# Performance work log

Hardware: AMD Instinct MI355X
Metric: run time of the kernel (lower is better)

## Reference

```python
import jax, jax.numpy as jnp
import numpy as np

B, T, C, H = 4, 2048, 1024, 16
D = C // H


def setup_inputs() -> dict:
    key = jax.random.key(0)
    ks = jax.random.split(key, 6)
    s = 1.0 / np.sqrt(C)
    return {
        "x": jax.random.normal(ks[0], (B, T, C), dtype=jnp.float32),
        "attention_mask": jnp.ones((B, 1, T), dtype=jnp.int32),
        "Wq": jax.random.normal(ks[1], (C, C), dtype=jnp.float32) * s,
        "bq": jnp.zeros((C,), dtype=jnp.float32),
        "Wk": jax.random.normal(ks[2], (C, C), dtype=jnp.float32) * s,
        "bk": jnp.zeros((C,), dtype=jnp.float32),
        "Wv": jax.random.normal(ks[3], (C, C), dtype=jnp.float32) * s,
        "bv": jnp.zeros((C,), dtype=jnp.float32),
        "Wp": jax.random.normal(ks[4], (C, C), dtype=jnp.float32) * s,
        "bp": jnp.zeros((C,), dtype=jnp.float32),
    }


def reference(x, attention_mask, Wq, bq, Wk, bk, Wv, bv, Wp, bp):
    b, t, c = x.shape
    d = c // H
    # projections (torch Linear: x @ W^T + b)
    q = (x @ Wq.T + bq).reshape(b, t, H, d).transpose(0, 2, 1, 3)  # [B,H,T,D]
    k = (x @ Wk.T + bk).reshape(b, t, H, d).transpose(0, 2, 1, 3)
    v = (x @ Wv.T + bv).reshape(b, t, H, d).transpose(0, 2, 1, 3)
    attn = jnp.einsum("bhqd,bhkd->bhqk", q, k) / jnp.sqrt(jnp.asarray(d, x.dtype))
    mask = attention_mask[:, :, :t]  # [B,1,T] -> broadcast over [B,H,T,T] keys
    attn = jnp.where(mask[:, :, None, :] == 0, jnp.asarray(-jnp.inf, x.dtype), attn)
    attn = jax.nn.softmax(attn, axis=-1)  # dropout p=0 (eval)
    y = jnp.einsum("bhqk,bhkd->bhqd", attn, v)
    y = y.transpose(0, 2, 1, 3).reshape(b, t, c)
    return y @ Wp.T + bp
```

## Files before the change

### kernel.cpp

```cpp
#include <hip/hip_runtime.h>


#define TT 2048
#define CC 1024
#define HH 16
#define DD 64
#define BB 4

typedef unsigned short u16;
typedef unsigned int u32;
typedef __attribute__((ext_vector_type(8))) short bf16x8;
typedef __attribute__((ext_vector_type(4))) float f32x4;
typedef __attribute__((ext_vector_type(4))) u32 u32x4;

#if __has_builtin(__builtin_amdgcn_exp2f)
#define EXP2(x) __builtin_amdgcn_exp2f(x)
#else
#define EXP2(x) __expf((x) * 0.6931471805599453f)
#endif

__device__ __forceinline__ u16 f2bf(float f) {
    u32 u = __builtin_bit_cast(u32, f);
    u += 0x7FFFu + ((u >> 16) & 1u);
    return (u16)(u >> 16);
}
__device__ __forceinline__ u32 pk2(float a, float b) {
    u32 ua = __builtin_bit_cast(u32, a); ua += 0x7FFFu + ((ua >> 16) & 1u);
    u32 ub = __builtin_bit_cast(u32, b); ub += 0x7FFFu + ((ub >> 16) & 1u);
    return __builtin_amdgcn_perm(ub, ua, 0x07060302);
}
__device__ __forceinline__ u32 cvtpk(float lo, float hi) {
    u32 r;
    asm("v_cvt_pk_bf16_f32 %0, %1, %2" : "=v"(r) : "v"(lo), "v"(hi));
    return r;
}

#define GLDS(g, l) __builtin_amdgcn_global_load_lds( \
    (const __attribute__((address_space(1))) void*)(g), \
    (__attribute__((address_space(3))) void*)(l), 16, 0, 0)

#define PH_SYNC() { __builtin_amdgcn_sched_barrier(0); \
                    __builtin_amdgcn_s_barrier(); \
                    __builtin_amdgcn_sched_barrier(0); }

__global__ __launch_bounds__(256) void wcvt(const float* __restrict__ s,
                                            u16* __restrict__ d, int n8) {
    const int i = blockIdx.x * 256 + threadIdx.x;
    if (i < n8) {
        const float4 f0 = ((const float4*)s)[2 * i];
        const float4 f1 = ((const float4*)s)[2 * i + 1];
        uint4 w;
        w.x = pk2(f0.x, f0.y); w.y = pk2(f0.z, f0.w);
        w.z = pk2(f1.x, f1.y); w.w = pk2(f1.z, f1.w);
        ((uint4*)d)[i] = w;
    }
}

__global__ __launch_bounds__(256) void wcvtA(const float* __restrict__ x,
                                             const float* __restrict__ Wq,
                                             const float* __restrict__ Wk,
                                             const float* __restrict__ Wv,
                                             u16* __restrict__ xb,
                                             u16* __restrict__ Wq16,
                                             u16* __restrict__ Wk16,
                                             u16* __restrict__ Wv16) {
    const int bid = blockIdx.x;
    const float* s; u16* d; int i;
    if (bid < 4096) {
        s = x; d = xb; i = bid * 256 + threadIdx.x;
    } else {
        const int t = bid - 4096;
        const int which = t >> 9, sub = t & 511;
        s = (which == 0) ? Wq : (which == 1) ? Wk : Wv;
        d = (which == 0) ? Wq16 : (which == 1) ? Wk16 : Wv16;
        i = sub * 256 + threadIdx.x;
    }
    const float4 f0 = ((const float4*)s)[2 * i];
    const float4 f1 = ((const float4*)s)[2 * i + 1];
    uint4 w;
    w.x = pk2(f0.x, f0.y); w.y = pk2(f0.z, f0.w);
    w.z = pk2(f1.x, f1.y); w.w = pk2(f1.z, f1.w);
    ((uint4*)d)[i] = w;
}

__global__ __launch_bounds__(512) void gemm8p(const u16* __restrict__ Ag,
                                              const u16* __restrict__ Wb,
                                              const float* __restrict__ b0,
                                              const float* __restrict__ b1,
                                              const float* __restrict__ b2,
                                              u16* __restrict__ outQ,
                                              u16* __restrict__ outK,
                                              u16* __restrict__ outV) {
    extern __shared__ u16 lds[];
    const int tid  = threadIdx.x;
    const int wave = tid >> 6, lane = tid & 63;
    const int quad = lane >> 4, l16 = lane & 15;
    const int wr = wave >> 2, wc = wave & 3;
    constexpr int NT = CC / 64;

    const int bid0 = blockIdx.y * 12 + blockIdx.x;
    const int bid  = (bid0 & 7) * 48 + (bid0 >> 3);
    const int bn = (bid % 12) * 256, bm = (bid / 12) * 256;

    u32 aOff[4], bOff[4]; int dstOff[4];
#pragma unroll
    for (int g = 0; g < 4; g++) {
        const int c = g * 512 + tid;
        const int row = c >> 3;
        const int kc = (c & 7) ^ (row & 7);
        aOff[g] = (u32)(bm + row) * CC + kc * 8;
        bOff[g] = (u32)(bn + row) * CC + kc * 8;
        dstOff[g] = c * 8;
    }

    int aO[8], bO[4];
#pragma unroll
    for (int i = 0; i < 8; i++) {
        const int row = wr * 128 + i * 16 + l16;
        aO[i] = row * 64 + (quad ^ (row & 7)) * 8;
    }
#pragma unroll
    for (int j = 0; j < 4; j++) {
        const int row = wc * 64 + j * 16 + l16;
        bO[j] = row * 64 + (quad ^ (row & 7)) * 8;
    }

    f32x4 acc[8][4] = {};

    {
        u16* An = lds;
        u16* Bn = lds + 32768;
        GLDS(&Ag[(size_t)aOff[0]], &An[dstOff[0]]);
        GLDS(&Ag[(size_t)aOff[2]], &An[dstOff[2]]);
#pragma unroll
        for (int g = 0; g < 4; g++) GLDS(&Wb[(size_t)bOff[g]], &Bn[dstOff[g]]);
        GLDS(&Ag[(size_t)aOff[1]], &An[dstOff[1]]);
        GLDS(&Ag[(size_t)aOff[3]], &An[dstOff[3]]);
        asm volatile("s_waitcnt vmcnt(2)" ::: "memory");
        PH_SYNC();
    }

#pragma unroll 1
    for (int t = 0; t < NT; t++) {
        const u16* Ab = lds + (t & 1) * 16384;
        const u16* Bb = lds + 32768 + (t & 1) * 16384;
        u16* An = lds + ((t & 1) ^ 1) * 16384;
        u16* Bn = lds + 32768 + ((t & 1) ^ 1) * 16384;
        const int k1 = (t + 1) * 64;
        const bool pf = (t + 1 < NT);

        bf16x8 af[4], bfr[4];

#pragma unroll
        for (int j = 0; j < 4; j++) bfr[j] = *(const bf16x8*)&Bb[bO[j]];
#pragma unroll
        for (int i = 0; i < 4; i++) af[i] = *(const bf16x8*)&Ab[aO[i]];
        asm volatile("s_waitcnt lgkmcnt(0)" ::: "memory");
        __builtin_amdgcn_sched_barrier(0);
        __builtin_amdgcn_s_setprio(1);
#pragma unroll
        for (int i = 0; i < 4; i++)
#pragma unroll
            for (int j = 0; j < 4; j++)
                acc[i][j] = __builtin_amdgcn_mfma_f32_16x16x32_bf16(af[i], bfr[j], acc[i][j], 0, 0, 0);
        __builtin_amdgcn_s_setprio(0);
        asm volatile("s_waitcnt vmcnt(0)" ::: "memory");
        PH_SYNC();

        if (pf) {
            GLDS(&Ag[(size_t)aOff[0] + k1], &An[dstOff[0]]);
            GLDS(&Ag[(size_t)aOff[2] + k1], &An[dstOff[2]]);
        }
#pragma unroll
        for (int i = 0; i < 4; i++) af[i] = *(const bf16x8*)&Ab[aO[4 + i]];
        asm volatile("s_waitcnt lgkmcnt(0)" ::: "memory");
        __builtin_amdgcn_sched_barrier(0);
        __builtin_amdgcn_s_setprio(1);
#pragma unroll
        for (int i = 0; i < 4; i++)
#pragma unroll
            for (int j = 0; j < 4; j++)
                acc[4 + i][j] = __builtin_amdgcn_mfma_f32_16x16x32_bf16(af[i], bfr[j], acc[4 + i][j], 0, 0, 0);
        __builtin_amdgcn_s_setprio(0);
        PH_SYNC();

        if (pf) {
#pragma unroll
            for (int g = 0; g < 4; g++)
                GLDS(&Wb[(size_t)bOff[g] + k1], &Bn[dstOff[g]]);
        }
#pragma unroll
        for (int j = 0; j < 4; j++) bfr[j] = *(const bf16x8*)&Bb[bO[j] ^ 32];
#pragma unroll
        for (int i = 0; i < 4; i++) af[i] = *(const bf16x8*)&Ab[aO[i] ^ 32];
        asm volatile("s_waitcnt lgkmcnt(0)" ::: "memory");
        __builtin_amdgcn_sched_barrier(0);
        __builtin_amdgcn_s_setprio(1);
#pragma unroll
        for (int i = 0; i < 4; i++)
#pragma unroll
            for (int j = 0; j < 4; j++)
                acc[i][j] = __builtin_amdgcn_mfma_f32_16x16x32_bf16(af[i], bfr[j], acc[i][j], 0, 0, 0);
        __builtin_amdgcn_s_setprio(0);
        PH_SYNC();

        if (pf) {
            GLDS(&Ag[(size_t)aOff[1] + k1], &An[dstOff[1]]);
            GLDS(&Ag[(size_t)aOff[3] + k1], &An[dstOff[3]]);
        }
#pragma unroll
        for (int i = 0; i < 4; i++) af[i] = *(const bf16x8*)&Ab[aO[4 + i] ^ 32];
        asm volatile("s_waitcnt lgkmcnt(0)" ::: "memory");
        __builtin_amdgcn_sched_barrier(0);
        __builtin_amdgcn_s_setprio(1);
#pragma unroll
        for (int i = 0; i < 4; i++)
#pragma unroll
            for (int j = 0; j < 4; j++)
                acc[4 + i][j] = __builtin_amdgcn_mfma_f32_16x16x32_bf16(af[i], bfr[j], acc[4 + i][j], 0, 0, 0);
        __builtin_amdgcn_s_setprio(0);
        if (pf) asm volatile("s_waitcnt vmcnt(2)" ::: "memory");
        else    asm volatile("s_waitcnt vmcnt(0)" ::: "memory");
        PH_SYNC();
    }

    const int mid = bn >> 10;
    const float* bias = (mid == 0) ? b0 : (mid == 1) ? b1 : b2;
#pragma unroll
    for (int j = 0; j < 4; j++) {
        const int col  = bn + wc * 64 + j * 16 + l16;
        const int colL = col & (CC - 1);
        const float bv = bias[colL];
#pragma unroll
        for (int i = 0; i < 8; i++) {
            const int row0 = bm + wr * 128 + i * 16 + quad * 4;
            if (mid < 2) {
                u16* out = mid ? outK : outQ;
#pragma unroll
                for (int r = 0; r < 4; r++)
                    out[(size_t)(row0 + r) * CC + colL] = f2bf(acc[i][j][r] + bv);
            } else {
                const int hh = colL >> 6, dch = colL & 63;
                const int bb = row0 >> 11, t0 = row0 & (TT - 1);
                const size_t idx = (((size_t)bb * HH + hh) * DD + dch) * TT + t0;
                uint2 w;
                w.x = pk2(acc[i][j][0] + bv, acc[i][j][1] + bv);
                w.y = pk2(acc[i][j][2] + bv, acc[i][j][3] + bv);
                *(uint2*)&outV[idx] = w;
            }
        }
    }
}

template <int BN, int WM, int WN, int MODE>
__global__ __launch_bounds__(512, 4) void gemmT(const u16* __restrict__ Ag,
                                                const u16* __restrict__ Bg,
                                                const float* __restrict__ b0,
                                                float* __restrict__ outF) {
    constexpr int NI = WM / 16, NJ = WN / 16;
    constexpr int WAVES_N = BN / WN;
    constexpr int BUFSZ = (256 + BN) * 32;
    constexpr int SPT = 2 + BN / 128;
    constexpr int NT = CC / 32;

    extern __shared__ u16 lds[];
    const int tid  = threadIdx.x;
    const int wave = tid >> 6, lane = tid & 63;
    const int quad = lane >> 4, l16 = lane & 15;
    const int wr = wave / WAVES_N, wc = wave & (WAVES_N - 1);

    constexpr int NBX = 1024 / BN;
    const int bid0 = blockIdx.y * NBX + blockIdx.x;
    const int chunk = (NBX * 32) >> 3;
    const int bid  = (bid0 & 7) * chunk + (bid0 >> 3);
    const int bn = (bid % NBX) * BN, bm = (bid / NBX) * 256;

    u32 aOff[2]; int aDst[2];
#pragma unroll
    for (int g = 0; g < 2; g++) {
        const int c = g * 512 + tid;
        const int row = c >> 2;
        const int kc = (c & 3) ^ ((row >> 1) & 3);
        aOff[g] = (u32)(bm + row) * CC + kc * 8;
        aDst[g] = c * 8;
    }
    u32 bOff[BN / 128]; int bDst[BN / 128];
#pragma unroll
    for (int g = 0; g < BN / 128; g++) {
        const int c = g * 512 + tid;
        const int row = c >> 2;
        const int kc = (c & 3) ^ ((row >> 1) & 3);
        bOff[g] = (u32)(bn + row) * CC + kc * 8;
        bDst[g] = 8192 + c * 8;
    }

    int aRd[NI], bRd[NJ];
#pragma unroll
    for (int i = 0; i < NI; i++) {
        const int row = wr * WM + i * 16 + l16;
        aRd[i] = row * 32 + (quad ^ ((row >> 1) & 3)) * 8;
    }
#pragma unroll
    for (int j = 0; j < NJ; j++) {
        const int row = wc * WN + j * 16 + l16;
        bRd[j] = 8192 + row * 32 + (quad ^ ((row >> 1) & 3)) * 8;
    }

    f32x4 acc[NI][NJ] = {};

#define STAGE_T(t)                                                        \
    {                                                                     \
        u16* dst = &lds[((t) % 3) * BUFSZ];                               \
        const int k0 = (t) * 32;                                          \
        _Pragma("unroll")                                                 \
        for (int g = 0; g < 2; g++)                                       \
            GLDS(&Ag[(size_t)aOff[g] + k0], &dst[aDst[g]]);               \
        _Pragma("unroll")                                                 \
        for (int g = 0; g < BN / 128; g++)                                \
            GLDS(&Bg[(size_t)bOff[g] + k0], &dst[bDst[g]]);               \
    }

#define COMPUTE_T(t)                                                      \
    {                                                                     \
        const u16* buf = &lds[((t) % 3) * BUFSZ];                         \
        bf16x8 af[NI], bfr[NJ];                                           \
        _Pragma("unroll")                                                 \
        for (int i = 0; i < NI; i++) af[i] = *(const bf16x8*)&buf[aRd[i]];\
        _Pragma("unroll")                                                 \
        for (int j = 0; j < NJ; j++) bfr[j] = *(const bf16x8*)&buf[bRd[j]];\
        __builtin_amdgcn_s_setprio(1);                                    \
        _Pragma("unroll")                                                 \
        for (int i = 0; i < NI; i++)                                      \
            _Pragma("unroll")                                             \
            for (int j = 0; j < NJ; j++)                                  \
                acc[i][j] = __builtin_amdgcn_mfma_f32_16x16x32_bf16(      \
                    af[i], bfr[j], acc[i][j], 0, 0, 0);                   \
        __builtin_amdgcn_s_setprio(0);                                    \
    }

#define WAIT_MAIN()                                                       \
    if constexpr (SPT == 3) asm volatile("s_waitcnt vmcnt(3)" ::: "memory"); \
    else                    asm volatile("s_waitcnt vmcnt(4)" ::: "memory");

    STAGE_T(0); STAGE_T(1);
    WAIT_MAIN();
    PH_SYNC();

#pragma unroll 1
    for (int t = 0; t < NT - 2; t++) {
        STAGE_T(t + 2);
        COMPUTE_T(t);
        WAIT_MAIN();
        PH_SYNC();
    }
    COMPUTE_T(NT - 2);
    asm volatile("s_waitcnt vmcnt(0)" ::: "memory");
    PH_SYNC();
    COMPUTE_T(NT - 1);

#undef STAGE_T
#undef COMPUTE_T
#undef WAIT_MAIN

#pragma unroll
    for (int j = 0; j < NJ; j++) {
        const int col = bn + wc * WN + j * 16 + l16;
        const float bv = b0[col];
#pragma unroll
        for (int i = 0; i < NI; i++) {
            const int row0 = bm + wr * WM + i * 16 + quad * 4;
#pragma unroll
            for (int r = 0; r < 4; r++)
                outF[(size_t)(row0 + r) * CC + col] = acc[i][j][r] + bv;
        }
    }
}

__global__ __launch_bounds__(512) void attn(const u16* __restrict__ Q,
                                            const u16* __restrict__ Kb,
                                            const u16* __restrict__ Vt,
                                            const int* __restrict__ mask,
                                            u16* __restrict__ Y) {
    const int b = blockIdx.z, h = blockIdx.y, qt = blockIdx.x;
    const int tid  = threadIdx.x;
    const int wave = tid >> 6, lane = tid & 63;
    const int quad = lane >> 4, l16 = lane & 15;
    const int qrow0 = qt * 256 + wave * 32;

    __shared__ u16 Ks[2][64 * 64];
    __shared__ u16 Vs[2][64 * 64];
    __shared__ __align__(16) float bias_lds[TT];

    const size_t qb = ((size_t)b * TT + qrow0) * CC + h * DD;

    bf16x8 qf[2][2];
#pragma unroll
    for (int m = 0; m < 2; m++)
#pragma unroll
        for (int ks = 0; ks < 2; ks++)
            qf[m][ks] = *(const bf16x8*)&Q[qb + (size_t)(m * 16 + l16) * CC + ks * 32 + quad * 8];

    {
        const int i = tid * 4;
        const int4 m0 = *(const int4*)&mask[b * TT + i];
        bias_lds[i + 0] = m0.x ? 0.f : -1e38f;
        bias_lds[i + 1] = m0.y ? 0.f : -1e38f;
        bias_lds[i + 2] = m0.z ? 0.f : -1e38f;
        bias_lds[i + 3] = m0.w ? 0.f : -1e38f;
    }

    const int c0 = tid;
    const int r0 = c0 >> 3;
    const int kp0 = (c0 & 7) ^ ((((r0 >> 3) & 1) << 2) | (r0 & 3));
    const int vp0 = (c0 & 7) ^ (r0 & 7);
    const u16* kgp = Kb + ((size_t)b * TT) * CC + h * DD;
    const u16* vgp = Vt + ((size_t)(b * HH + h) * DD) * TT;

    const int rowA = ((l16 >> 2) << 3) | (l16 & 3);
    const int s0k  = (((l16 >> 2) & 1) << 2) | (l16 & 3);

    f32x4 o[2][4] = {};
    float lsum[2] = {};
    const float SC = 0.18033688011112042f;

    GLDS(&kgp[(size_t)r0 * CC + kp0 * 8], &Ks[0][c0 * 8]);
    GLDS(&vgp[(size_t)r0 * TT + vp0 * 8], &Vs[0][c0 * 8]);
    asm volatile("s_waitcnt vmcnt(0) lgkmcnt(0)" ::: "memory");
    __builtin_amdgcn_s_barrier();
    __builtin_amdgcn_sched_barrier(0);

#pragma unroll 1
    for (int kt = 0; kt < TT; kt += 64) {
        const int cur = (kt >> 6) & 1;
        const u16* Kc = &Ks[cur][0];
        const u16* Vc = &Vs[cur][0];

        if (kt + 64 < TT) {
            const int nxt = cur ^ 1;
            GLDS(&kgp[(size_t)(kt + 64 + r0) * CC + kp0 * 8], &Ks[nxt][c0 * 8]);
            GLDS(&vgp[(size_t)r0 * TT + kt + 64 + vp0 * 8], &Vs[nxt][c0 * 8]);
        }

        const f32x4 bA = *(const f32x4*)&bias_lds[kt + quad * 8];
        const f32x4 bB = *(const f32x4*)&bias_lds[kt + quad * 8 + 4];
        const f32x4 bC = *(const f32x4*)&bias_lds[kt + 32 + quad * 8];
        const f32x4 bD = *(const f32x4*)&bias_lds[kt + 32 + quad * 8 + 4];

        f32x4 s2[2][4] = {};
        __builtin_amdgcn_s_setprio(1);
#pragma unroll
        for (int n = 0; n < 4; n++) {
            const int rowK = rowA + (n & 1) * 4 + (n >> 1) * 32;
#pragma unroll
            for (int ks = 0; ks < 2; ks++) {
                const int pos = ((ks << 2) + quad) ^ s0k;
                const bf16x8 kf = *(const bf16x8*)&Kc[rowK * 64 + pos * 8];
#pragma unroll
                for (int m = 0; m < 2; m++)
                    s2[m][n] = __builtin_amdgcn_mfma_f32_16x16x32_bf16(kf, qf[m][ks], s2[m][n], 0, 0, 0);
            }
        }
        __builtin_amdgcn_s_setprio(0);

#pragma unroll
        for (int ks = 0; ks < 2; ks++) {
            bf16x8 pf[2];
#pragma unroll
            for (int m = 0; m < 2; m++) {
                u32 pw[4];
#pragma unroll
                for (int nn = 0; nn < 2; nn++) {
                    const int n = 2 * ks + nn;
                    const f32x4 bv = (n == 0) ? bA : (n == 1) ? bB : (n == 2) ? bC : bD;
                    const float p0 = EXP2(fmaf(s2[m][n][0], SC, bv[0]));
                    const float p1 = EXP2(fmaf(s2[m][n][1], SC, bv[1]));
                    const float p2 = EXP2(fmaf(s2[m][n][2], SC, bv[2]));
                    const float p3 = EXP2(fmaf(s2[m][n][3], SC, bv[3]));
                    lsum[m] += (p0 + p1) + (p2 + p3);
                    pw[2 * nn]     = cvtpk(p0, p1);
                    pw[2 * nn + 1] = cvtpk(p2, p3);
                }
                const u32x4 t = { pw[0], pw[1], pw[2], pw[3] };
                pf[m] = __builtin_bit_cast(bf16x8, t);
            }
            __builtin_amdgcn_s_setprio(1);
#pragma unroll
            for (int dt = 0; dt < 4; dt++) {
                const int vrow = dt * 16 + l16;
                const int pos = ((ks << 2) + quad) ^ (vrow & 7);
                const bf16x8 vf = *(const bf16x8*)&Vc[vrow * 64 + pos * 8];
#pragma unroll
                for (int m = 0; m < 2; m++)
                    o[m][dt] = __builtin_amdgcn_mfma_f32_16x16x32_bf16(pf[m], vf, o[m][dt], 0, 0, 0);
            }
            __builtin_amdgcn_s_setprio(0);
        }

        asm volatile("s_waitcnt vmcnt(0)" ::: "memory");
        __builtin_amdgcn_sched_barrier(0);
        __builtin_amdgcn_s_barrier();
    }

#pragma unroll
    for (int m = 0; m < 2; m++) {
        lsum[m] += __shfl_xor(lsum[m], 16, 64);
        lsum[m] += __shfl_xor(lsum[m], 32, 64);
    }

#pragma unroll
    for (int m = 0; m < 2; m++) {
        float inv[4];
#pragma unroll
        for (int r = 0; r < 4; r++)
            inv[r] = 1.0f / __shfl(lsum[m], quad * 4 + r, 64);
#pragma unroll
        for (int dt = 0; dt < 4; dt++)
#pragma unroll
            for (int r = 0; r < 4; r++)
                Y[qb + (size_t)(m * 16 + quad * 4 + r) * CC + dt * 16 + l16] = f2bf(o[m][dt][r] * inv[r]);
    }
}

extern "C" void kernel_launch(void* const* d_in, const int* in_sizes, int n_in,
                              void* d_out, int out_size, void* d_ws, size_t ws_size,
                              hipStream_t stream) {
    const float* x    = (const float*)d_in[0];
    const int*   mask = (const int*)d_in[1];
    const float* Wq   = (const float*)d_in[2];
    const float* bq   = (const float*)d_in[3];
    const float* Wk   = (const float*)d_in[4];
    const float* bk   = (const float*)d_in[5];
    const float* Wv   = (const float*)d_in[6];
    const float* bv   = (const float*)d_in[7];
    const float* Wp   = (const float*)d_in[8];
    const float* bp   = (const float*)d_in[9];

    u16* ws = (u16*)d_ws;
    const size_t sz = (size_t)BB * TT * CC;
    u16* Qb   = ws;
    u16* Kbuf = ws + sz;
    u16* Vtb  = ws + 2 * sz;

    u16* xb   = (u16*)d_out;
    u16* Wq16 = xb + sz;
    u16* Wk16 = Wq16 + (size_t)CC * CC;
    u16* Wv16 = Wk16 + (size_t)CC * CC;

    static bool inited = false;
    if (!inited) {
        (void)hipFuncSetAttribute((const void*)gemm8p,
                                  hipFuncAttributeMaxDynamicSharedMemorySize, 131072);
        (void)hipFuncSetAttribute((const void*)gemmT<128, 64, 64, 1>,
                                  hipFuncAttributeMaxDynamicSharedMemorySize, 73728);
        inited = true;
    }

    const int W8 = CC * CC / 8;

    wcvtA<<<5632, 256, 0, stream>>>(x, Wq, Wk, Wv, xb, Wq16, Wk16, Wv16);

    gemm8p<<<dim3(12, 32), 512, 131072, stream>>>(
        xb, Wq16, bq, bk, bv, Qb, Kbuf, Vtb);

    attn<<<dim3(TT / 256, HH, BB), 512, 0, stream>>>(Qb, Kbuf, Vtb, mask, Qb);

    wcvt<<<512, 256, 0, stream>>>(Wp, Kbuf, W8);

    gemmT<128, 64, 64, 1><<<dim3(8, 32), 512, 73728, stream>>>(
        Qb, Kbuf, bp, (float*)d_out);
}
```

Before: 291.1 us.

## Issue QKV GEMM prefetch at iteration start and shrink output-projection tile

The fused QKV GEMM now issues all next-tile global-to-LDS loads at the start of each K iteration instead of spreading them across four phases. It waits for them all only at the end of the iteration. The output-projection GEMM is generalized with a BM parameter and launched with 128x128 tiles (512 blocks, 48KB LDS) instead of 256x128 (256 blocks). This gives more blocks for occupancy and load balance on the final projection, at the cost of less data reuse per block. Issuing the prefetch in one burst may also change the overlap with MFMA work.

```diff
diff --git a/kernel.cpp b/kernel.cpp
--- a/kernel.cpp
+++ b/kernel.cpp
@@ -83,7 +83,7 @@
     ((uint4*)d)[i] = w;
 }
 
-__global__ __launch_bounds__(512) void gemm8p(const u16* __restrict__ Ag,
+__global__ __launch_bounds__(512) void gemm4p(const u16* __restrict__ Ag,
                                               const u16* __restrict__ Wb,
                                               const float* __restrict__ b0,
                                               const float* __restrict__ b1,
@@ -130,13 +130,11 @@
     {
         u16* An = lds;
         u16* Bn = lds + 32768;
-        GLDS(&Ag[(size_t)aOff[0]], &An[dstOff[0]]);
-        GLDS(&Ag[(size_t)aOff[2]], &An[dstOff[2]]);
+#pragma unroll
+        for (int g = 0; g < 4; g++) GLDS(&Ag[(size_t)aOff[g]], &An[dstOff[g]]);
 #pragma unroll
         for (int g = 0; g < 4; g++) GLDS(&Wb[(size_t)bOff[g]], &Bn[dstOff[g]]);
-        GLDS(&Ag[(size_t)aOff[1]], &An[dstOff[1]]);
-        GLDS(&Ag[(size_t)aOff[3]], &An[dstOff[3]]);
-        asm volatile("s_waitcnt vmcnt(2)" ::: "memory");
+        asm volatile("s_waitcnt vmcnt(0)" ::: "memory");
         PH_SYNC();
     }
 
@@ -151,6 +149,14 @@
 
         bf16x8 af[4], bfr[4];
 
+        if (pf) {
+#pragma unroll
+            for (int g = 0; g < 4; g++)
+                GLDS(&Ag[(size_t)aOff[g] + k1], &An[dstOff[g]]);
+#pragma unroll
+            for (int g = 0; g < 4; g++)
+                GLDS(&Wb[(size_t)bOff[g] + k1], &Bn[dstOff[g]]);
+        }
 #pragma unroll
         for (int j = 0; j < 4; j++) bfr[j] = *(const bf16x8*)&Bb[bO[j]];
 #pragma unroll
@@ -164,13 +170,8 @@
             for (int j = 0; j < 4; j++)
                 acc[i][j] = __builtin_amdgcn_mfma_f32_16x16x32_bf16(af[i], bfr[j], acc[i][j], 0, 0, 0);
         __builtin_amdgcn_s_setprio(0);
-        asm volatile("s_waitcnt vmcnt(0)" ::: "memory");
         PH_SYNC();
 
-        if (pf) {
-            GLDS(&Ag[(size_t)aOff[0] + k1], &An[dstOff[0]]);
-            GLDS(&Ag[(size_t)aOff[2] + k1], &An[dstOff[2]]);
-        }
 #pragma unroll
         for (int i = 0; i < 4; i++) af[i] = *(const bf16x8*)&Ab[aO[4 + i]];
         asm volatile("s_waitcnt lgkmcnt(0)" ::: "memory");
@@ -184,11 +185,6 @@
         __builtin_amdgcn_s_setprio(0);
         PH_SYNC();
 
-        if (pf) {
-#pragma unroll
-            for (int g = 0; g < 4; g++)
-                GLDS(&Wb[(size_t)bOff[g] + k1], &Bn[dstOff[g]]);
-        }
 #pragma unroll
         for (int j = 0; j < 4; j++) bfr[j] = *(const bf16x8*)&Bb[bO[j] ^ 32];
 #pragma unroll
@@ -204,10 +200,6 @@
         __builtin_amdgcn_s_setprio(0);
         PH_SYNC();
 
-        if (pf) {
-            GLDS(&Ag[(size_t)aOff[1] + k1], &An[dstOff[1]]);
-            GLDS(&Ag[(size_t)aOff[3] + k1], &An[dstOff[3]]);
-        }
 #pragma unroll
         for (int i = 0; i < 4; i++) af[i] = *(const bf16x8*)&Ab[aO[4 + i] ^ 32];
         asm volatile("s_waitcnt lgkmcnt(0)" ::: "memory");
@@ -219,8 +211,7 @@
             for (int j = 0; j < 4; j++)
                 acc[4 + i][j] = __builtin_amdgcn_mfma_f32_16x16x32_bf16(af[i], bfr[j], acc[4 + i][j], 0, 0, 0);
         __builtin_amdgcn_s_setprio(0);
-        if (pf) asm volatile("s_waitcnt vmcnt(2)" ::: "memory");
-        else    asm volatile("s_waitcnt vmcnt(0)" ::: "memory");
+        asm volatile("s_waitcnt vmcnt(0)" ::: "memory");
         PH_SYNC();
     }
 
@@ -252,46 +243,49 @@
     }
 }
 
-template <int BN, int WM, int WN, int MODE>
+template <int BM, int BN, int WM, int WN>
 __global__ __launch_bounds__(512, 4) void gemmT(const u16* __restrict__ Ag,
                                                 const u16* __restrict__ Bg,
                                                 const float* __restrict__ b0,
                                                 float* __restrict__ outF) {
     constexpr int NI = WM / 16, NJ = WN / 16;
     constexpr int WAVES_N = BN / WN;
-    constexpr int BUFSZ = (256 + BN) * 32;
-    constexpr int SPT = 2 + BN / 128;
+    constexpr int BOFF = BM * 32;
+    constexpr int BUFSZ = (BM + BN) * 32;
+    constexpr int AG = BM / 128, BG = BN / 128;
+    constexpr int SPT = AG + BG;
     constexpr int NT = CC / 32;
+    constexpr int NBX = 1024 / BN;
+    constexpr int NBY = 8192 / BM;
 
     extern __shared__ u16 lds[];
     const int tid  = threadIdx.x;
     const int wave = tid >> 6, lane = tid & 63;
     const int quad = lane >> 4, l16 = lane & 15;
-    const int wr = wave / WAVES_N, wc = wave & (WAVES_N - 1);
-
-    constexpr int NBX = 1024 / BN;
+    const int wr = wave / WAVES_N, wc = wave % WAVES_N;
+
     const int bid0 = blockIdx.y * NBX + blockIdx.x;
-    const int chunk = (NBX * 32) >> 3;
+    const int chunk = (NBX * NBY) >> 3;
     const int bid  = (bid0 & 7) * chunk + (bid0 >> 3);
-    const int bn = (bid % NBX) * BN, bm = (bid / NBX) * 256;
-
-    u32 aOff[2]; int aDst[2];
-#pragma unroll
-    for (int g = 0; g < 2; g++) {
+    const int bn = (bid % NBX) * BN, bm = (bid / NBX) * BM;
+
+    u32 aOff[AG]; int aDst[AG];
+#pragma unroll
+    for (int g = 0; g < AG; g++) {
         const int c = g * 512 + tid;
         const int row = c >> 2;
         const int kc = (c & 3) ^ ((row >> 1) & 3);
         aOff[g] = (u32)(bm + row) * CC + kc * 8;
         aDst[g] = c * 8;
     }
-    u32 bOff[BN / 128]; int bDst[BN / 128];
-#pragma unroll
-    for (int g = 0; g < BN / 128; g++) {
+    u32 bOff[BG]; int bDst[BG];
+#pragma unroll
+    for (int g = 0; g < BG; g++) {
         const int c = g * 512 + tid;
         const int row = c >> 2;
         const int kc = (c & 3) ^ ((row >> 1) & 3);
         bOff[g] = (u32)(bn + row) * CC + kc * 8;
-        bDst[g] = 8192 + c * 8;
+        bDst[g] = BOFF + c * 8;
     }
 
     int aRd[NI], bRd[NJ];
@@ -303,7 +297,7 @@
 #pragma unroll
     for (int j = 0; j < NJ; j++) {
         const int row = wc * WN + j * 16 + l16;
-        bRd[j] = 8192 + row * 32 + (quad ^ ((row >> 1) & 3)) * 8;
+        bRd[j] = BOFF + row * 32 + (quad ^ ((row >> 1) & 3)) * 8;
     }
 
     f32x4 acc[NI][NJ] = {};
@@ -313,10 +307,10 @@
         u16* dst = &lds[((t) % 3) * BUFSZ];                               \
         const int k0 = (t) * 32;                                          \
         _Pragma("unroll")                                                 \
-        for (int g = 0; g < 2; g++)                                       \
+        for (int g = 0; g < AG; g++)                                      \
             GLDS(&Ag[(size_t)aOff[g] + k0], &dst[aDst[g]]);               \
         _Pragma("unroll")                                                 \
-        for (int g = 0; g < BN / 128; g++)                                \
+        for (int g = 0; g < BG; g++)                                      \
             GLDS(&Bg[(size_t)bOff[g] + k0], &dst[bDst[g]]);               \
     }
 
@@ -339,8 +333,9 @@
     }
 
 #define WAIT_MAIN()                                                       \
-    if constexpr (SPT == 3) asm volatile("s_waitcnt vmcnt(3)" ::: "memory"); \
-    else                    asm volatile("s_waitcnt vmcnt(4)" ::: "memory");
+    if constexpr (SPT == 2) asm volatile("s_waitcnt vmcnt(2)" ::: "memory"); \
+    else if constexpr (SPT == 3) asm volatile("s_waitcnt vmcnt(3)" ::: "memory"); \
+    else asm volatile("s_waitcnt vmcnt(4)" ::: "memory");
 
     STAGE_T(0); STAGE_T(1);
     WAIT_MAIN();
@@ -548,10 +543,10 @@
 
     static bool inited = false;
     if (!inited) {
-        (void)hipFuncSetAttribute((const void*)gemm8p,
+        (void)hipFuncSetAttribute((const void*)gemm4p,
                                   hipFuncAttributeMaxDynamicSharedMemorySize, 131072);
-        (void)hipFuncSetAttribute((const void*)gemmT<128, 64, 64, 1>,
-                                  hipFuncAttributeMaxDynamicSharedMemorySize, 73728);
+        (void)hipFuncSetAttribute((const void*)gemmT<128, 128, 32, 64>,
+                                  hipFuncAttributeMaxDynamicSharedMemorySize, 49152);
         inited = true;
     }
 
@@ -559,13 +554,13 @@
 
     wcvtA<<<5632, 256, 0, stream>>>(x, Wq, Wk, Wv, xb, Wq16, Wk16, Wv16);
 
-    gemm8p<<<dim3(12, 32), 512, 131072, stream>>>(
+    gemm4p<<<dim3(12, 32), 512, 131072, stream>>>(
         xb, Wq16, bq, bk, bv, Qb, Kbuf, Vtb);
 
     attn<<<dim3(TT / 256, HH, BB), 512, 0, stream>>>(Qb, Kbuf, Vtb, mask, Qb);
 
     wcvt<<<512, 256, 0, stream>>>(Wp, Kbuf, W8);
 
-    gemmT<128, 64, 64, 1><<<dim3(8, 32), 512, 73728, stream>>>(
+    gemmT<128, 128, 32, 64><<<dim3(8, 64), 512, 49152, stream>>>(
         Qb, Kbuf, bp, (float*)d_out);
 }
```

New measurement: 286.6 us. No clear change (-1.6%).
